# Kernel optimization log

Measured on AMD Instinct MI355X. Metric: run time of the kernel, lower is better.

Reference implementation:

```python
import jax, jax.numpy as jnp
import numpy as np


def _grid_mesh(n):
    ys, xs = np.meshgrid(np.arange(n), np.arange(n), indexing='ij')
    verts = np.stack([xs, ys, np.zeros_like(xs)], -1).reshape(-1, 3).astype(np.float32) / (n - 1)
    idx = np.arange(n * n).reshape(n, n)
    v00 = idx[:-1, :-1].ravel(); v01 = idx[:-1, 1:].ravel()
    v10 = idx[1:, :-1].ravel(); v11 = idx[1:, 1:].ravel()
    faces = np.concatenate([np.stack([v00, v10, v01], 1), np.stack([v01, v10, v11], 1)], 0).astype(np.int32)
    e = np.concatenate([faces[:, [0, 1]], faces[:, [1, 2]], faces[:, [2, 0]]], 0)
    e = np.unique(np.sort(e, axis=1), axis=0).astype(np.int32)
    return verts, faces, e


def setup_inputs() -> dict:
    N_GRID, B, S = 200, 2, 5000
    verts_np, faces_np, edges_np = _grid_mesh(N_GRID)
    verts_np[:, 2] = 0.1 * np.sin(2 * np.pi * verts_np[:, 0]) * np.sin(2 * np.pi * verts_np[:, 1])
    key = jax.random.key(0)
    k1, k2, k3, k4 = jax.random.split(key, 4)
    verts_std = jnp.asarray(verts_np)
    verts_scr = verts_std[None] + 5e-4 * jax.random.normal(k1, (B,) + verts_std.shape, jnp.float32)
    xy = jax.random.uniform(k2, (B, S, 2), jnp.float32)
    z = 0.1 * jnp.sin(2 * jnp.pi * xy[..., 0]) * jnp.sin(2 * jnp.pi * xy[..., 1])
    trg_points = jnp.concatenate([xy, z[..., None]], -1)
    rand_face_u = jax.random.uniform(k3, (B, S), jnp.float32)
    rand_bary = jax.random.uniform(k4, (B, S, 2), jnp.float32)
    return {
        'verts_scr': verts_scr,
        'verts_std': verts_std,
        'trg_points': trg_points,
        'rand_face_u': rand_face_u,
        'rand_bary': rand_bary,
        'faces': jnp.asarray(faces_np),
        'edges': jnp.asarray(edges_np),
    }


def _cot_edges(verts, faces):
    # pytorch3d cot_laplacian: per-face cotangents, symmetrized edge list (6F entries).
    v0, v1, v2 = verts[faces[:, 0]], verts[faces[:, 1]], verts[faces[:, 2]]
    A = jnp.linalg.norm(v1 - v2, axis=1)
    B = jnp.linalg.norm(v0 - v2, axis=1)
    C = jnp.linalg.norm(v0 - v1, axis=1)
    A2, B2, C2 = A * A, B * B, C * C
    s = 0.5 * (A + B + C)
    area = jnp.sqrt(jnp.clip(s * (s - A) * (s - B) * (s - C), 1e-12, None))
    cot = jnp.stack([B2 + C2 - A2, A2 + C2 - B2, A2 + B2 - C2], axis=1) / (4.0 * area[:, None])
    ii = faces[:, jnp.array([1, 2, 0])].reshape(-1)
    jj = faces[:, jnp.array([2, 0, 1])].reshape(-1)
    src = jnp.concatenate([ii, jj])
    dst = jnp.concatenate([jj, ii])
    w = jnp.concatenate([cot.reshape(-1), cot.reshape(-1)])
    return src, dst, w


def _sample_points(verts, faces, u_face, r_bary):
    # area-weighted face sampling + pytorch3d barycentric coords
    v0, v1, v2 = verts[faces[:, 0]], verts[faces[:, 1]], verts[faces[:, 2]]
    areas = 0.5 * jnp.linalg.norm(jnp.cross(v1 - v0, v2 - v0), axis=1)
    cdf = jnp.cumsum(areas) / jnp.sum(areas)
    fidx = jnp.clip(jnp.searchsorted(cdf, u_face), 0, faces.shape[0] - 1)
    su = jnp.sqrt(r_bary[:, 0])
    w0, w1, w2 = 1.0 - su, su * (1.0 - r_bary[:, 1]), su * r_bary[:, 1]
    return w0[:, None] * v0[fidx] + w1[:, None] * v1[fidx] + w2[:, None] * v2[fidx]


def _chamfer(x, y):
    # squared-distance chamfer, mean over points then batch (pytorch3d defaults)
    d = (jnp.sum(x * x, -1)[:, :, None] + jnp.sum(y * y, -1)[:, None, :]
         - 2.0 * jnp.einsum('bsd,btd->bst', x, y))
    return jnp.min(d, 2).mean() + jnp.min(d, 1).mean()


def _forward(verts_scr, verts_std, trg_points, rand_face_u, rand_bary, faces, edges):
    Vn = verts_std.shape[0]
    # chamfer between sampled src surface points and target point cloud
    sample_scr = jax.vmap(lambda v, u, r: _sample_points(v, faces, u, r))(verts_scr, rand_face_u, rand_bary)
    loss_p0 = _chamfer(sample_scr, trg_points)
    loss_n1 = jnp.asarray(1e-5, verts_scr.dtype)  # tensor-target branch

    # cot laplacian smoothing (method='cot')
    def lap_one(v):
        src, dst, w = _cot_edges(v, faces)
        Lv = jax.ops.segment_sum(w[:, None] * v[dst], src, num_segments=Vn)
        rw = jax.ops.segment_sum(w, src, num_segments=Vn)
        inv = jnp.where(rw > 0, 1.0 / jnp.maximum(rw, 1e-12), 0.0)
        return jnp.linalg.norm(Lv * inv[:, None] - v, axis=1).mean()

    loss_lap = jax.vmap(lap_one)(verts_scr).mean()

    # edge loss against mean edge length of the std mesh
    target_len = jnp.linalg.norm(verts_std[edges[:, 0]] - verts_std[edges[:, 1]], axis=1).mean()
    elen = jnp.linalg.norm(verts_scr[:, edges[:, 0]] - verts_scr[:, edges[:, 1]], axis=-1)
    loss_edge = ((elen - target_len) ** 2).mean()

    # ARAP rigid loss on std-mesh cot connectivity/weights
    src, dst, w = _cot_edges(verts_std, faces)
    e_std = verts_std[src] - verts_std[dst]

    def rigid_one(v):
        e_scr = v[src] - v[dst]
        S = jax.ops.segment_sum(w[:, None, None] * e_std[:, :, None] * e_scr[:, None, :], src, num_segments=Vn)
        U, _, Vt = jnp.linalg.svd(S)
        R = jnp.matmul(jnp.swapaxes(Vt, -1, -2), jnp.swapaxes(U, -1, -2))
        flip = jnp.where(jnp.linalg.det(R) < 0, -1.0, 1.0)
        Vt2 = Vt.at[:, -1, :].multiply(flip[:, None])
        R = jnp.matmul(jnp.swapaxes(Vt2, -1, -2), jnp.swapaxes(U, -1, -2))
        res = e_scr - jnp.einsum('eij,ej->ei', R[src], e_std)
        return jax.ops.segment_sum(w * jnp.sum(res * res, 1), src, num_segments=Vn)

    loss_rigid = jax.vmap(rigid_one)(verts_scr).mean()
    return jnp.stack([loss_p0, loss_n1, loss_lap, loss_edge, loss_rigid])


def reference(verts_scr, verts_std, trg_points, rand_face_u, rand_bary, faces, edges):
    return _forward(verts_scr, verts_std, trg_points, rand_face_u, rand_bary, faces, edges)
```

## Files before the change

### kernel.cpp

```cpp
#include <hip/hip_runtime.h>
#include <math.h>

#define TPB 256
#define MAXDEG 8

static __device__ __forceinline__ void atomAddD(double* p, double v) {
  __hip_atomic_fetch_add(p, v, __ATOMIC_RELAXED, __HIP_MEMORY_SCOPE_AGENT);
}

static __device__ __forceinline__ double bredsum(double v) {
  __shared__ double sb[TPB];
  int t = threadIdx.x;
  sb[t] = v;
  __syncthreads();
  for (int o = TPB / 2; o > 0; o >>= 1) {
    if (t < o) sb[t] += sb[t + o];
    __syncthreads();
  }
  double r = sb[0];
  __syncthreads();
  return r;
}

template <int p, int q, int r>
static __device__ __forceinline__ void jrot(double A[3][3], double V[3][3]) {
  double apq = A[p][q];
  if (apq == 0.0) return;
  double app = A[p][p], aqq = A[q][q];
  double theta = (aqq - app) / (2.0 * apq);
  double t = 1.0 / (fabs(theta) + sqrt(theta * theta + 1.0));
  if (theta < 0.0) t = -t;
  double c = 1.0 / sqrt(t * t + 1.0), sn = t * c;
  A[p][p] = app - t * apq;
  A[q][q] = aqq + t * apq;
  A[p][q] = 0.0;
  A[q][p] = 0.0;
  double arp = A[r][p], arq = A[r][q];
  A[r][p] = c * arp - sn * arq; A[p][r] = A[r][p];
  A[r][q] = sn * arp + c * arq; A[q][r] = A[r][q];
#pragma unroll
  for (int k = 0; k < 3; k++) {
    double vkp = V[k][p], vkq = V[k][q];
    V[k][p] = c * vkp - sn * vkq;
    V[k][q] = sn * vkp + c * vkq;
  }
}

#define ESWAP(la, lax, lay, laz, lb, lbx, lby, lbz)                       \
  if (la < lb) {                                                          \
    double t_;                                                            \
    t_ = la; la = lb; lb = t_;                                            \
    t_ = lax; lax = lbx; lbx = t_;                                        \
    t_ = lay; lay = lby; lby = t_;                                        \
    t_ = laz; laz = lbz; lbz = t_;                                        \
  }

static __device__ void kabschR(const double S[3][3], double R9[9]) {
  double A[3][3];
#pragma unroll
  for (int a = 0; a < 3; a++)
#pragma unroll
    for (int c = 0; c < 3; c++)
      A[a][c] = S[0][a] * S[0][c] + S[1][a] * S[1][c] + S[2][a] * S[2][c];
  double V[3][3] = {{1, 0, 0}, {0, 1, 0}, {0, 0, 1}};
  for (int sw = 0; sw < 12; sw++) {
    double off = fabs(A[0][1]) + fabs(A[0][2]) + fabs(A[1][2]);
    double dia = fabs(A[0][0]) + fabs(A[1][1]) + fabs(A[2][2]);
    if (!(off > dia * 1e-15)) break;
    jrot<0, 1, 2>(A, V);
    jrot<0, 2, 1>(A, V);
    jrot<1, 2, 0>(A, V);
  }
  double l0 = A[0][0], l1 = A[1][1], l2 = A[2][2];
  double a0x = V[0][0], a0y = V[1][0], a0z = V[2][0];
  double a1x = V[0][1], a1y = V[1][1], a1z = V[2][1];
  double a2x = V[0][2], a2y = V[1][2], a2z = V[2][2];
  ESWAP(l0, a0x, a0y, a0z, l1, a1x, a1y, a1z);
  ESWAP(l0, a0x, a0y, a0z, l2, a2x, a2y, a2z);
  ESWAP(l1, a1x, a1y, a1z, l2, a2x, a2y, a2z);
  double R00 = 1, R01 = 0, R02 = 0, R10 = 0, R11 = 1, R12 = 0, R20 = 0, R21 = 0, R22 = 1;
  double b1x = S[0][0] * a0x + S[0][1] * a0y + S[0][2] * a0z;
  double b1y = S[1][0] * a0x + S[1][1] * a0y + S[1][2] * a0z;
  double b1z = S[2][0] * a0x + S[2][1] * a0y + S[2][2] * a0z;
  double b2x = S[0][0] * a1x + S[0][1] * a1y + S[0][2] * a1z;
  double b2y = S[1][0] * a1x + S[1][1] * a1y + S[1][2] * a1z;
  double b2z = S[2][0] * a1x + S[2][1] * a1y + S[2][2] * a1z;
  double n1 = sqrt(b1x * b1x + b1y * b1y + b1z * b1z);
  if (n1 > 1e-300 && isfinite(n1)) {
    double u1x = b1x / n1, u1y = b1y / n1, u1z = b1z / n1;
    double dp = u1x * b2x + u1y * b2y + u1z * b2z;
    b2x -= dp * u1x; b2y -= dp * u1y; b2z -= dp * u1z;
    double n2 = sqrt(b2x * b2x + b2y * b2y + b2z * b2z);
    double u2x, u2y, u2z;
    if (n2 > n1 * 1e-14) {
      u2x = b2x / n2; u2y = b2y / n2; u2z = b2z / n2;
    } else {
      double f0 = fabs(u1x), f1 = fabs(u1y), f2 = fabs(u1z);
      double e0, e1, e2;
      if (f0 <= f1 && f0 <= f2) { e0 = 1.0 - u1x * u1x; e1 = -u1x * u1y; e2 = -u1x * u1z; }
      else if (f1 <= f2)        { e0 = -u1y * u1x; e1 = 1.0 - u1y * u1y; e2 = -u1y * u1z; }
      else                      { e0 = -u1z * u1x; e1 = -u1z * u1y; e2 = 1.0 - u1z * u1z; }
      double nw = sqrt(e0 * e0 + e1 * e1 + e2 * e2);
      u2x = e0 / nw; u2y = e1 / nw; u2z = e2 / nw;
    }
    double u3x = u1y * u2z - u1z * u2y;
    double u3y = u1z * u2x - u1x * u2z;
    double u3z = u1x * u2y - u1y * u2x;
    double w3x = a0y * a1z - a0z * a1y;
    double w3y = a0z * a1x - a0x * a1z;
    double w3z = a0x * a1y - a0y * a1x;
    R00 = a0x * u1x + a1x * u2x + w3x * u3x;
    R01 = a0x * u1y + a1x * u2y + w3x * u3y;
    R02 = a0x * u1z + a1x * u2z + w3x * u3z;
    R10 = a0y * u1x + a1y * u2x + w3y * u3x;
    R11 = a0y * u1y + a1y * u2y + w3y * u3y;
    R12 = a0y * u1z + a1y * u2z + w3y * u3z;
    R20 = a0z * u1x + a1z * u2x + w3z * u3x;
    R21 = a0z * u1y + a1z * u2y + w3z * u3y;
    R22 = a0z * u1z + a1z * u2z + w3z * u3z;
  }
  R9[0] = R00; R9[1] = R01; R9[2] = R02;
  R9[3] = R10; R9[4] = R11; R9[5] = R12;
  R9[6] = R20; R9[7] = R21; R9[8] = R22;
}

static __device__ __forceinline__ double resid(const double* R, const double* es,
                                               const double* ec) {
  double r0 = ec[0] - (R[0] * es[0] + R[1] * es[1] + R[2] * es[2]);
  double r1 = ec[1] - (R[3] * es[0] + R[4] * es[1] + R[5] * es[2]);
  double r2 = ec[2] - (R[6] * es[0] + R[7] * es[1] + R[8] * es[2]);
  return r0 * r0 + r1 * r1 + r2 * r2;
}

__global__ void kInitRowmin(unsigned* rm, int n) {
  int i = blockIdx.x * blockDim.x + threadIdx.x;
  if (i < n) rm[i] = 0x7f800000u;
}

__global__ void kFacePrep(const float* verts, const float* vstd, const int* faces,
                          double* areas, double* ccot, double* scot,
                          int B, int Vn, int F) {
  int i = blockIdx.x * blockDim.x + threadIdx.x;
  if (i >= B * F) return;
  int b = i / F, f = i % F;
  const float* vb = verts + (size_t)b * Vn * 3;
  int i0 = faces[f * 3], i1 = faces[f * 3 + 1], i2 = faces[f * 3 + 2];
  {
    double p0x = vb[i0 * 3], p0y = vb[i0 * 3 + 1], p0z = vb[i0 * 3 + 2];
    double p1x = vb[i1 * 3], p1y = vb[i1 * 3 + 1], p1z = vb[i1 * 3 + 2];
    double p2x = vb[i2 * 3], p2y = vb[i2 * 3 + 1], p2z = vb[i2 * 3 + 2];
    double ax = p1x - p0x, ay = p1y - p0y, az = p1z - p0z;
    double bx = p2x - p0x, by = p2y - p0y, bz = p2z - p0z;
    double cx = ay * bz - az * by, cy = az * bx - ax * bz, cz = ax * by - ay * bx;
    areas[i] = 0.5 * sqrt(cx * cx + cy * cy + cz * cz);
    double dx = p1x - p2x, dy = p1y - p2y, dz = p1z - p2z;
    double A2 = dx * dx + dy * dy + dz * dz;
    double B2 = bx * bx + by * by + bz * bz;
    double C2 = ax * ax + ay * ay + az * az;
    double A = sqrt(A2), Bl = sqrt(B2), C = sqrt(C2);
    double s = 0.5 * (A + Bl + C);
    double pr = s * (s - A) * (s - Bl) * (s - C);
    pr = pr < 1e-12 ? 1e-12 : pr;
    double inv4 = 1.0 / (4.0 * sqrt(pr));
    ccot[(size_t)i * 3 + 0] = (B2 + C2 - A2) * inv4;
    ccot[(size_t)i * 3 + 1] = (A2 + C2 - B2) * inv4;
    ccot[(size_t)i * 3 + 2] = (A2 + B2 - C2) * inv4;
  }
  if (b == 0) {
    double p0x = vstd[i0 * 3], p0y = vstd[i0 * 3 + 1], p0z = vstd[i0 * 3 + 2];
    double p1x = vstd[i1 * 3], p1y = vstd[i1 * 3 + 1], p1z = vstd[i1 * 3 + 2];
    double p2x = vstd[i2 * 3], p2y = vstd[i2 * 3 + 1], p2z = vstd[i2 * 3 + 2];
    double ax = p1x - p0x, ay = p1y - p0y, az = p1z - p0z;
    double bx = p2x - p0x, by = p2y - p0y, bz = p2z - p0z;
    double dx = p1x - p2x, dy = p1y - p2y, dz = p1z - p2z;
    double A2 = dx * dx + dy * dy + dz * dz;
    double B2 = bx * bx + by * by + bz * bz;
    double C2 = ax * ax + ay * ay + az * az;
    double A = sqrt(A2), Bl = sqrt(B2), C = sqrt(C2);
    double s = 0.5 * (A + Bl + C);
    double pr = s * (s - A) * (s - Bl) * (s - C);
    pr = pr < 1e-12 ? 1e-12 : pr;
    double inv4 = 1.0 / (4.0 * sqrt(pr));
    scot[(size_t)f * 3 + 0] = (B2 + C2 - A2) * inv4;
    scot[(size_t)f * 3 + 1] = (A2 + C2 - B2) * inv4;
    scot[(size_t)f * 3 + 2] = (A2 + B2 - C2) * inv4;
  }
}

__global__ void kScan1(double* a, double* bsum, int F, int nc) {
  int blk = blockIdx.x;
  int b = blk / nc, c = blk % nc;
  int t = threadIdx.x;
  int f = c * 1024 + t;
  __shared__ double s[1024];
  double v = (f < F) ? a[(size_t)b * F + f] : 0.0;
  s[t] = v;
  __syncthreads();
  for (int o = 1; o < 1024; o <<= 1) {
    double ad = (t >= o) ? s[t - o] : 0.0;
    __syncthreads();
    s[t] += ad;
    __syncthreads();
  }
  if (f < F) a[(size_t)b * F + f] = s[t];
  if (t == 1023) bsum[(size_t)b * nc + c] = s[1023];
}

__global__ void kScan2(const double* bsum, double* boffs, int nc) {
  int b = blockIdx.x, t = threadIdx.x;
  __shared__ double s[1024];
  double v = (t < nc) ? bsum[(size_t)b * nc + t] : 0.0;
  s[t] = v;
  __syncthreads();
  for (int o = 1; o < 1024; o <<= 1) {
    double ad = (t >= o) ? s[t - o] : 0.0;
    __syncthreads();
    s[t] += ad;
    __syncthreads();
  }
  if (t < nc) boffs[(size_t)b * nc + t] = s[t] - v;
}

__global__ void kScan3(double* a, const double* boffs, int F, int nc) {
  int blk = blockIdx.x;
  int b = blk / nc, c = blk % nc;
  int f = c * 1024 + threadIdx.x;
  if (f < F) a[(size_t)b * F + f] += boffs[(size_t)b * nc + c];
}

__global__ void kSample(const float* verts, const int* faces, const double* cdf,
                        const float* rfu, const float* rbary, float* samples,
                        int B, int Vn, int F, int S) {
  int i = blockIdx.x * blockDim.x + threadIdx.x;
  if (i >= B * S) return;
  int b = i / S;
  const double* c = cdf + (size_t)b * F;
  double total = c[F - 1];
  double tgt = (double)rfu[i] * total;
  int lo = 0, hi = F;
  while (lo < hi) {
    int m = (lo + hi) >> 1;
    if (c[m] < tgt) lo = m + 1; else hi = m;
  }
  int f = lo < F ? lo : F - 1;
  const float* vb = verts + (size_t)b * Vn * 3;
  int i0 = faces[f * 3], i1 = faces[f * 3 + 1], i2 = faces[f * 3 + 2];
  float r0 = rbary[(size_t)i * 2], r1 = rbary[(size_t)i * 2 + 1];
  float su = sqrtf(r0);
  float w0 = 1.f - su, w1 = su * (1.f - r1), w2 = su * r1;
  samples[(size_t)i * 3 + 0] = w0 * vb[i0 * 3 + 0] + w1 * vb[i1 * 3 + 0] + w2 * vb[i2 * 3 + 0];
  samples[(size_t)i * 3 + 1] = w0 * vb[i0 * 3 + 1] + w1 * vb[i1 * 3 + 1] + w2 * vb[i2 * 3 + 1];
  samples[(size_t)i * 3 + 2] = w0 * vb[i0 * 3 + 2] + w1 * vb[i1 * 3 + 2] + w2 * vb[i2 * 3 + 2];
}

__global__ void kChamfer(const float* X, const float* Y, unsigned* rowmin, int S) {
  int b = blockIdx.z;
  int i = blockIdx.x * TPB + threadIdx.x;
  int j0 = blockIdx.y * TPB;
  int n = min(TPB, S - j0);
  __shared__ float4 sy[TPB];
  const float* Yb = Y + ((size_t)b * S + j0) * 3;
  if ((int)threadIdx.x < n) {
    int t = threadIdx.x;
    sy[t] = make_float4(Yb[t * 3], Yb[t * 3 + 1], Yb[t * 3 + 2], 0.f);
  }
  __syncthreads();
  if (i >= S) return;
  const float* Xb = X + (size_t)b * S * 3;
  float x0 = Xb[i * 3], x1 = Xb[i * 3 + 1], x2 = Xb[i * 3 + 2];
  float inf = __int_as_float(0x7f800000);
  float m0 = inf, m1 = inf, m2 = inf, m3 = inf;
  int k = 0;
  for (; k + 4 <= n; k += 4) {
    float4 y0 = sy[k], y1 = sy[k + 1], y2 = sy[k + 2], y3 = sy[k + 3];
    float a0 = x0 - y0.x, b0 = x1 - y0.y, c0 = x2 - y0.z;
    float a1 = x0 - y1.x, b1 = x1 - y1.y, c1 = x2 - y1.z;
    float a2 = x0 - y2.x, b2 = x1 - y2.y, c2 = x2 - y2.z;
    float a3 = x0 - y3.x, b3 = x1 - y3.y, c3 = x2 - y3.z;
    m0 = fminf(m0, a0 * a0 + b0 * b0 + c0 * c0);
    m1 = fminf(m1, a1 * a1 + b1 * b1 + c1 * c1);
    m2 = fminf(m2, a2 * a2 + b2 * b2 + c2 * c2);
    m3 = fminf(m3, a3 * a3 + b3 * b3 + c3 * c3);
  }
  for (; k < n; k++) {
    float4 y = sy[k];
    float a = x0 - y.x, bb = x1 - y.y, cc = x2 - y.z;
    m0 = fminf(m0, a * a + bb * bb + cc * cc);
  }
  float mn = fminf(fminf(m0, m1), fminf(m2, m3));
  atomicMin(&rowmin[(size_t)b * S + i], __float_as_uint(mn));
}

__global__ void kReduceRowmin(const unsigned* rm, int n, double* acc) {
  int i = blockIdx.x * TPB + threadIdx.x;
  double v = 0.0;
  if (i < n) v = (double)__uint_as_float(rm[i]);
  double r = bredsum(v);
  if (threadIdx.x == 0) atomAddD(acc, r);
}

__global__ void kEdgeStd(const float* vstd, const int* edges, int E, double* acc) {
  int i = blockIdx.x * TPB + threadIdx.x;
  double val = 0.0;
  if (i < E) {
    int e0 = edges[(size_t)i * 2], e1 = edges[(size_t)i * 2 + 1];
    double dx = (double)vstd[e0 * 3 + 0] - vstd[e1 * 3 + 0];
    double dy = (double)vstd[e0 * 3 + 1] - vstd[e1 * 3 + 1];
    double dz = (double)vstd[e0 * 3 + 2] - vstd[e1 * 3 + 2];
    val = sqrt(dx * dx + dy * dy + dz * dz);
  }
  double r = bredsum(val);
  if (threadIdx.x == 0) atomAddD(acc, r);
}

__global__ void kEdgeLoss(const float* vscr, const int* edges, int B, int Vn, int E,
                          const double* tacc, double* acc) {
  int i = blockIdx.x * TPB + threadIdx.x;
  double tl = tacc[0] / (double)E;
  double val = 0.0;
  if (i < B * E) {
    int b = i / E, e = i % E;
    const float* vb = vscr + (size_t)b * Vn * 3;
    int e0 = edges[(size_t)e * 2], e1 = edges[(size_t)e * 2 + 1];
    double dx = (double)vb[e0 * 3 + 0] - vb[e1 * 3 + 0];
    double dy = (double)vb[e0 * 3 + 1] - vb[e1 * 3 + 1];
    double dz = (double)vb[e0 * 3 + 2] - vb[e1 * 3 + 2];
    double l = sqrt(dx * dx + dy * dy + dz * dz);
    double d = l - tl;
    val = d * d;
  }
  double r = bredsum(val);
  if (threadIdx.x == 0) atomAddD(acc, r);
}

__global__ void kAdjFill(const int* faces, int* cnt, int4* adjtab, int F) {
  int f = blockIdx.x * TPB + threadIdx.x;
  if (f >= F) return;
  int j0 = faces[f * 3], j1 = faces[f * 3 + 1], j2 = faces[f * 3 + 2];
  int f3 = f * 3;
  int s0 = atomicAdd(&cnt[j0], 1);
  if (s0 < MAXDEG) adjtab[(size_t)j0 * MAXDEG + s0] = make_int4(j1, j2, f3 + 1, f3 + 2);
  int s1 = atomicAdd(&cnt[j1], 1);
  if (s1 < MAXDEG) adjtab[(size_t)j1 * MAXDEG + s1] = make_int4(j2, j0, f3 + 2, f3 + 0);
  int s2 = atomicAdd(&cnt[j2], 1);
  if (s2 < MAXDEG) adjtab[(size_t)j2 * MAXDEG + s2] = make_int4(j0, j1, f3 + 0, f3 + 1);
}

__global__ void kVertexLapR(const float* vstd, const float* vscr,
                            const int* cnt, const int4* adjtab, const double* scot,
                            const double* ccot, double* Rmat, int B, int Vn, int F,
                            double* accLap) {
  int idx = blockIdx.x * TPB + threadIdx.x;
  double vlap = 0.0;
  if (idx < B * Vn) {
    int b = idx / Vn, v = idx % Vn;
    const float* cb = vscr + (size_t)b * Vn * 3;
    const double* ccb = ccot + (size_t)b * F * 3;
    double pasx = vstd[v * 3], pasy = vstd[v * 3 + 1], pasz = vstd[v * 3 + 2];
    double pacx = cb[v * 3], pacy = cb[v * 3 + 1], pacz = cb[v * 3 + 2];
    int n = cnt[v];
    if (n > MAXDEG) n = MAXDEG;
    const int4* at = adjtab + (size_t)v * MAXDEG;
    double S00 = 0, S01 = 0, S02 = 0, S10 = 0, S11 = 0, S12 = 0, S20 = 0, S21 = 0, S22 = 0;
    double Lx = 0, Ly = 0, Lz = 0, rw = 0;
    for (int k = 0; k < n; k++) {
      int4 e = at[k];
      int jb = e.x, jc = e.y;
      double cBs = scot[e.z], cCs = scot[e.w];
      double cBc = ccb[e.z], cCc = ccb[e.w];
      double pbsx = vstd[jb * 3], pbsy = vstd[jb * 3 + 1], pbsz = vstd[jb * 3 + 2];
      double pcsx = vstd[jc * 3], pcsy = vstd[jc * 3 + 1], pcsz = vstd[jc * 3 + 2];
      double pbcx = cb[jb * 3], pbcy = cb[jb * 3 + 1], pbcz = cb[jb * 3 + 2];
      double pccx = cb[jc * 3], pccy = cb[jc * 3 + 1], pccz = cb[jc * 3 + 2];
      Lx += cCc * pbcx + cBc * pccx;
      Ly += cCc * pbcy + cBc * pccy;
      Lz += cCc * pbcz + cBc * pccz;
      rw += cBc + cCc;
      double e1sx = pasx - pbsx, e1sy = pasy - pbsy, e1sz = pasz - pbsz;
      double e2sx = pasx - pcsx, e2sy = pasy - pcsy, e2sz = pasz - pcsz;
      double e1cx = pacx - pbcx, e1cy = pacy - pbcy, e1cz = pacz - pbcz;
      double e2cx = pacx - pccx, e2cy = pacy - pccy, e2cz = pacz - pccz;
      S00 += cCs * e1sx * e1cx + cBs * e2sx * e2cx;
      S01 += cCs * e1sx * e1cy + cBs * e2sx * e2cy;
      S02 += cCs * e1sx * e1cz + cBs * e2sx * e2cz;
      S10 += cCs * e1sy * e1cx + cBs * e2sy * e2cx;
      S11 += cCs * e1sy * e1cy + cBs * e2sy * e2cy;
      S12 += cCs * e1sy * e1cz + cBs * e2sy * e2cz;
      S20 += cCs * e1sz * e1cx + cBs * e2sz * e2cx;
      S21 += cCs * e1sz * e1cy + cBs * e2sz * e2cy;
      S22 += cCs * e1sz * e1cz + cBs * e2sz * e2cz;
    }
    double inv = (rw > 0.0) ? 1.0 / fmax(rw, 1e-12) : 0.0;
    double dx = Lx * inv - pacx, dy = Ly * inv - pacy, dz = Lz * inv - pacz;
    vlap = sqrt(dx * dx + dy * dy + dz * dz);
    double S[3][3] = {{S00, S01, S02}, {S10, S11, S12}, {S20, S21, S22}};
    double R9[9];
    kabschR(S, R9);
    double* rp = Rmat + (size_t)idx * 9;
#pragma unroll
    for (int r = 0; r < 9; r++) rp[r] = R9[r];
  }
  double r1 = bredsum(vlap);
  if (threadIdx.x == 0) atomAddD(accLap, r1);
}

__global__ void kRigidRes(const float* vstd, const float* vscr, const int* faces,
                          const double* scot, const double* Rmat, int B, int Vn, int F,
                          double* acc) {
  int i = blockIdx.x * TPB + threadIdx.x;
  double val = 0.0;
  if (i < B * F) {
    int b = i / F, f = i % F;
    int i0 = faces[f * 3], i1 = faces[f * 3 + 1], i2 = faces[f * 3 + 2];
    const float* cb = vscr + (size_t)b * Vn * 3;
    double cs0 = scot[(size_t)f * 3], cs1 = scot[(size_t)f * 3 + 1], cs2 = scot[(size_t)f * 3 + 2];
    double p0x = vstd[i0 * 3], p0y = vstd[i0 * 3 + 1], p0z = vstd[i0 * 3 + 2];
    double p1x = vstd[i1 * 3], p1y = vstd[i1 * 3 + 1], p1z = vstd[i1 * 3 + 2];
    double p2x = vstd[i2 * 3], p2y = vstd[i2 * 3 + 1], p2z = vstd[i2 * 3 + 2];
    double q0x = cb[i0 * 3], q0y = cb[i0 * 3 + 1], q0z = cb[i0 * 3 + 2];
    double q1x = cb[i1 * 3], q1y = cb[i1 * 3 + 1], q1z = cb[i1 * 3 + 2];
    double q2x = cb[i2 * 3], q2y = cb[i2 * 3 + 1], q2z = cb[i2 * 3 + 2];
    double e01s[3] = {p0x - p1x, p0y - p1y, p0z - p1z};
    double e02s[3] = {p0x - p2x, p0y - p2y, p0z - p2z};
    double e12s[3] = {p1x - p2x, p1y - p2y, p1z - p2z};
    double e01c[3] = {q0x - q1x, q0y - q1y, q0z - q1z};
    double e02c[3] = {q0x - q2x, q0y - q2y, q0z - q2z};
    double e12c[3] = {q1x - q2x, q1y - q2y, q1z - q2z};
    const double* R0 = Rmat + ((size_t)b * Vn + i0) * 9;
    const double* R1 = Rmat + ((size_t)b * Vn + i1) * 9;
    const double* R2 = Rmat + ((size_t)b * Vn + i2) * 9;
    val = cs1 * resid(R0, e02s, e02c) + cs2 * resid(R0, e01s, e01c)
        + cs0 * resid(R1, e12s, e12c) + cs2 * resid(R1, e01s, e01c)
        + cs1 * resid(R2, e02s, e02c) + cs0 * resid(R2, e12s, e12c);
  }
  double r = bredsum(val);
  if (threadIdx.x == 0) atomAddD(acc, r);
}

__global__ void kFinalize(const double* acc, float* out, int B, int Vn, int S, int E) {
  if (blockIdx.x == 0 && threadIdx.x == 0) {
    out[0] = (float)(acc[0] / ((double)B * S));
    out[1] = 1e-5f;
    out[2] = (float)(acc[1] / ((double)B * Vn));
    out[3] = (float)(acc[3] / ((double)B * E));
    out[4] = (float)(acc[4] / ((double)B * Vn));
  }
}

extern "C" void kernel_launch(void* const* d_in, const int* in_sizes, int n_in,
                              void* d_out, int out_size, void* d_ws, size_t ws_size,
                              hipStream_t stream) {
  const float* vscr = (const float*)d_in[0];
  const float* vstd = (const float*)d_in[1];
  const float* trg  = (const float*)d_in[2];
  const float* rfu  = (const float*)d_in[3];
  const float* rby  = (const float*)d_in[4];
  const int* faces  = (const int*)d_in[5];
  const int* edges  = (const int*)d_in[6];
  float* out = (float*)d_out;

  int nVs = in_sizes[1];
  int Vn = nVs / 3;
  int B = in_sizes[0] / nVs;
  int S = in_sizes[3] / B;
  int F = in_sizes[5] / 3;
  int E = in_sizes[6] / 2;
  int nc = (F + 1023) / 1024;

  char* p = (char*)d_ws;
  auto alloc = [&](size_t bytes) -> void* {
    void* r = (void*)p;
    p += (bytes + 255) & ~(size_t)255;
    return r;
  };
  double* cdf   = (double*)alloc((size_t)B * F * sizeof(double));
  double* bsum  = (double*)alloc((size_t)B * nc * sizeof(double));
  double* boffs = (double*)alloc((size_t)B * nc * sizeof(double));
  double* scot  = (double*)alloc((size_t)F * 3 * sizeof(double));
  double* ccot  = (double*)alloc((size_t)B * F * 3 * sizeof(double));
  double* Rmat  = (double*)alloc((size_t)B * Vn * 9 * sizeof(double));
  float* samples   = (float*)alloc((size_t)B * S * 3 * sizeof(float));
  unsigned* rowmin = (unsigned*)alloc((size_t)2 * B * S * sizeof(unsigned));
  int* adjcnt   = (int*)alloc((size_t)Vn * sizeof(int));
  int4* adjtab  = (int4*)alloc((size_t)Vn * MAXDEG * sizeof(int4));
  double* accum = (double*)alloc(8 * sizeof(double));

  hipMemsetAsync(adjcnt, 0, (size_t)Vn * sizeof(int), stream);
  hipMemsetAsync(accum, 0, 8 * sizeof(double), stream);

  int nrm = 2 * B * S;
  kInitRowmin<<<(nrm + TPB - 1) / TPB, TPB, 0, stream>>>(rowmin, nrm);

  kAdjFill<<<(F + TPB - 1) / TPB, TPB, 0, stream>>>(faces, adjcnt, adjtab, F);

  kFacePrep<<<(B * F + TPB - 1) / TPB, TPB, 0, stream>>>(vscr, vstd, faces, cdf, ccot,
                                                         scot, B, Vn, F);
  kScan1<<<B * nc, 1024, 0, stream>>>(cdf, bsum, F, nc);
  kScan2<<<B, 1024, 0, stream>>>(bsum, boffs, nc);
  kScan3<<<B * nc, 1024, 0, stream>>>(cdf, boffs, F, nc);
  kSample<<<(B * S + TPB - 1) / TPB, TPB, 0, stream>>>(vscr, faces, cdf, rfu, rby,
                                                       samples, B, Vn, F, S);
  dim3 cg((S + TPB - 1) / TPB, (S + TPB - 1) / TPB, B);
  kChamfer<<<cg, TPB, 0, stream>>>(samples, trg, rowmin, S);
  kChamfer<<<cg, TPB, 0, stream>>>(trg, samples, rowmin + (size_t)B * S, S);
  kReduceRowmin<<<(nrm + TPB - 1) / TPB, TPB, 0, stream>>>(rowmin, nrm, accum + 0);

  kEdgeStd<<<(E + TPB - 1) / TPB, TPB, 0, stream>>>(vstd, edges, E, accum + 2);
  kEdgeLoss<<<(B * E + TPB - 1) / TPB, TPB, 0, stream>>>(vscr, edges, B, Vn, E,
                                                         accum + 2, accum + 3);

  kVertexLapR<<<(B * Vn + TPB - 1) / TPB, TPB, 0, stream>>>(vstd, vscr, adjcnt, adjtab,
                                                            scot, ccot, Rmat, B, Vn, F,
                                                            accum + 1);
  kRigidRes<<<(B * F + TPB - 1) / TPB, TPB, 0, stream>>>(vstd, vscr, faces, scot,
                                                         Rmat, B, Vn, F, accum + 4);

  kFinalize<<<1, 1, 0, stream>>>(accum, out, B, Vn, S, E);
}
```

Baseline: 200.1 us.

## Fuse kernels to cut launch count: merged prep, single-pass scan, combined chamfer

Merges face prep, adjacency fill and std edge-length sum into one kernel. The three-kernel scan becomes a warp-shuffle scan where the last-arriving block computes the chunk offsets. Sampling then searches hierarchically over chunk totals and local prefixes instead of needing a globally fixed-up CDF. Both chamfer directions run in one launch, rowmin init becomes a memset, and the edge, reduce and finalize kernels are folded into others using a last-block counter. The aim is to remove launch overhead and serial small kernels, at the cost of atomic-counter logic and threadfence ordering that must be correct.

```diff
diff --git a/kernel.cpp b/kernel.cpp
--- a/kernel.cpp
+++ b/kernel.cpp
@@ -132,117 +132,169 @@
   return r0 * r0 + r1 * r1 + r2 * r2;
 }
 
-__global__ void kInitRowmin(unsigned* rm, int n) {
-  int i = blockIdx.x * blockDim.x + threadIdx.x;
-  if (i < n) rm[i] = 0x7f800000u;
-}
-
-__global__ void kFacePrep(const float* verts, const float* vstd, const int* faces,
-                          double* areas, double* ccot, double* scot,
-                          int B, int Vn, int F) {
-  int i = blockIdx.x * blockDim.x + threadIdx.x;
-  if (i >= B * F) return;
-  int b = i / F, f = i % F;
-  const float* vb = verts + (size_t)b * Vn * 3;
-  int i0 = faces[f * 3], i1 = faces[f * 3 + 1], i2 = faces[f * 3 + 2];
-  {
-    double p0x = vb[i0 * 3], p0y = vb[i0 * 3 + 1], p0z = vb[i0 * 3 + 2];
-    double p1x = vb[i1 * 3], p1y = vb[i1 * 3 + 1], p1z = vb[i1 * 3 + 2];
-    double p2x = vb[i2 * 3], p2y = vb[i2 * 3 + 1], p2z = vb[i2 * 3 + 2];
-    double ax = p1x - p0x, ay = p1y - p0y, az = p1z - p0z;
-    double bx = p2x - p0x, by = p2y - p0y, bz = p2z - p0z;
-    double cx = ay * bz - az * by, cy = az * bx - ax * bz, cz = ax * by - ay * bx;
-    areas[i] = 0.5 * sqrt(cx * cx + cy * cy + cz * cz);
-    double dx = p1x - p2x, dy = p1y - p2y, dz = p1z - p2z;
-    double A2 = dx * dx + dy * dy + dz * dz;
-    double B2 = bx * bx + by * by + bz * bz;
-    double C2 = ax * ax + ay * ay + az * az;
-    double A = sqrt(A2), Bl = sqrt(B2), C = sqrt(C2);
-    double s = 0.5 * (A + Bl + C);
-    double pr = s * (s - A) * (s - Bl) * (s - C);
-    pr = pr < 1e-12 ? 1e-12 : pr;
-    double inv4 = 1.0 / (4.0 * sqrt(pr));
-    ccot[(size_t)i * 3 + 0] = (B2 + C2 - A2) * inv4;
-    ccot[(size_t)i * 3 + 1] = (A2 + C2 - B2) * inv4;
-    ccot[(size_t)i * 3 + 2] = (A2 + B2 - C2) * inv4;
-  }
-  if (b == 0) {
-    double p0x = vstd[i0 * 3], p0y = vstd[i0 * 3 + 1], p0z = vstd[i0 * 3 + 2];
-    double p1x = vstd[i1 * 3], p1y = vstd[i1 * 3 + 1], p1z = vstd[i1 * 3 + 2];
-    double p2x = vstd[i2 * 3], p2y = vstd[i2 * 3 + 1], p2z = vstd[i2 * 3 + 2];
-    double ax = p1x - p0x, ay = p1y - p0y, az = p1z - p0z;
-    double bx = p2x - p0x, by = p2y - p0y, bz = p2z - p0z;
-    double dx = p1x - p2x, dy = p1y - p2y, dz = p1z - p2z;
-    double A2 = dx * dx + dy * dy + dz * dz;
-    double B2 = bx * bx + by * by + bz * bz;
-    double C2 = ax * ax + ay * ay + az * az;
-    double A = sqrt(A2), Bl = sqrt(B2), C = sqrt(C2);
-    double s = 0.5 * (A + Bl + C);
-    double pr = s * (s - A) * (s - Bl) * (s - C);
-    pr = pr < 1e-12 ? 1e-12 : pr;
-    double inv4 = 1.0 / (4.0 * sqrt(pr));
-    scot[(size_t)f * 3 + 0] = (B2 + C2 - A2) * inv4;
-    scot[(size_t)f * 3 + 1] = (A2 + C2 - B2) * inv4;
-    scot[(size_t)f * 3 + 2] = (A2 + B2 - C2) * inv4;
-  }
-}
-
-__global__ void kScan1(double* a, double* bsum, int F, int nc) {
+static __device__ __forceinline__ void heronCots(double A2, double B2, double C2,
+                                                 double* c0, double* c1, double* c2) {
+  double A = sqrt(A2), Bl = sqrt(B2), C = sqrt(C2);
+  double s = 0.5 * (A + Bl + C);
+  double pr = s * (s - A) * (s - Bl) * (s - C);
+  pr = pr < 1e-12 ? 1e-12 : pr;
+  double inv4 = 1.0 / (4.0 * sqrt(pr));
+  *c0 = (B2 + C2 - A2) * inv4;
+  *c1 = (A2 + C2 - B2) * inv4;
+  *c2 = (A2 + B2 - C2) * inv4;
+}
+
+__global__ void kPrep(const float* vscr, const float* vstd, const int* faces,
+                      const int* edges, double* cdf, double* ccot, double* scot,
+                      int* adjcnt, int4* adjtab, double* accEdgeStd,
+                      int B, int Vn, int F, int E) {
+  int i = blockIdx.x * TPB + threadIdx.x;
+  if (i < B * F) {
+    int b = i / F, f = i % F;
+    const float* vb = vscr + (size_t)b * Vn * 3;
+    int i0 = faces[f * 3], i1 = faces[f * 3 + 1], i2 = faces[f * 3 + 2];
+    {
+      double p0x = vb[i0 * 3], p0y = vb[i0 * 3 + 1], p0z = vb[i0 * 3 + 2];
+      double p1x = vb[i1 * 3], p1y = vb[i1 * 3 + 1], p1z = vb[i1 * 3 + 2];
+      double p2x = vb[i2 * 3], p2y = vb[i2 * 3 + 1], p2z = vb[i2 * 3 + 2];
+      double ax = p1x - p0x, ay = p1y - p0y, az = p1z - p0z;
+      double bx = p2x - p0x, by = p2y - p0y, bz = p2z - p0z;
+      double cx = ay * bz - az * by, cy = az * bx - ax * bz, cz = ax * by - ay * bx;
+      cdf[i] = 0.5 * sqrt(cx * cx + cy * cy + cz * cz);
+      double dx = p1x - p2x, dy = p1y - p2y, dz = p1z - p2z;
+      double A2 = dx * dx + dy * dy + dz * dz;
+      double B2 = bx * bx + by * by + bz * bz;
+      double C2 = ax * ax + ay * ay + az * az;
+      double c0, c1, c2;
+      heronCots(A2, B2, C2, &c0, &c1, &c2);
+      ccot[(size_t)i * 3 + 0] = c0;
+      ccot[(size_t)i * 3 + 1] = c1;
+      ccot[(size_t)i * 3 + 2] = c2;
+    }
+    if (b == 0) {
+      double p0x = vstd[i0 * 3], p0y = vstd[i0 * 3 + 1], p0z = vstd[i0 * 3 + 2];
+      double p1x = vstd[i1 * 3], p1y = vstd[i1 * 3 + 1], p1z = vstd[i1 * 3 + 2];
+      double p2x = vstd[i2 * 3], p2y = vstd[i2 * 3 + 1], p2z = vstd[i2 * 3 + 2];
+      double ax = p1x - p0x, ay = p1y - p0y, az = p1z - p0z;
+      double bx = p2x - p0x, by = p2y - p0y, bz = p2z - p0z;
+      double dx = p1x - p2x, dy = p1y - p2y, dz = p1z - p2z;
+      double A2 = dx * dx + dy * dy + dz * dz;
+      double B2 = bx * bx + by * by + bz * bz;
+      double C2 = ax * ax + ay * ay + az * az;
+      double c0, c1, c2;
+      heronCots(A2, B2, C2, &c0, &c1, &c2);
+      scot[(size_t)f * 3 + 0] = c0;
+      scot[(size_t)f * 3 + 1] = c1;
+      scot[(size_t)f * 3 + 2] = c2;
+      int f3 = f * 3;
+      int s0 = atomicAdd(&adjcnt[i0], 1);
+      if (s0 < MAXDEG) adjtab[(size_t)i0 * MAXDEG + s0] = make_int4(i1, i2, f3 + 1, f3 + 2);
+      int s1 = atomicAdd(&adjcnt[i1], 1);
+      if (s1 < MAXDEG) adjtab[(size_t)i1 * MAXDEG + s1] = make_int4(i2, i0, f3 + 2, f3 + 0);
+      int s2 = atomicAdd(&adjcnt[i2], 1);
+      if (s2 < MAXDEG) adjtab[(size_t)i2 * MAXDEG + s2] = make_int4(i0, i1, f3 + 0, f3 + 1);
+    }
+  }
+  double eval = 0.0;
+  if (i < E) {
+    int e0 = edges[(size_t)i * 2], e1 = edges[(size_t)i * 2 + 1];
+    double dx = (double)vstd[e0 * 3 + 0] - vstd[e1 * 3 + 0];
+    double dy = (double)vstd[e0 * 3 + 1] - vstd[e1 * 3 + 1];
+    double dz = (double)vstd[e0 * 3 + 2] - vstd[e1 * 3 + 2];
+    eval = sqrt(dx * dx + dy * dy + dz * dz);
+  }
+  double r = bredsum(eval);
+  if (threadIdx.x == 0) atomAddD(accEdgeStd, r);
+}
+
+__global__ void kScanFused(double* a, double* bsum, double* boffs, int F, int nc,
+                           int B, int* cnt) {
   int blk = blockIdx.x;
   int b = blk / nc, c = blk % nc;
-  int t = threadIdx.x;
+  int t = threadIdx.x, lane = t & 63, wid = t >> 6;
   int f = c * 1024 + t;
-  __shared__ double s[1024];
-  double v = (f < F) ? a[(size_t)b * F + f] : 0.0;
-  s[t] = v;
-  __syncthreads();
-  for (int o = 1; o < 1024; o <<= 1) {
-    double ad = (t >= o) ? s[t - o] : 0.0;
-    __syncthreads();
-    s[t] += ad;
-    __syncthreads();
-  }
-  if (f < F) a[(size_t)b * F + f] = s[t];
-  if (t == 1023) bsum[(size_t)b * nc + c] = s[1023];
-}
-
-__global__ void kScan2(const double* bsum, double* boffs, int nc) {
-  int b = blockIdx.x, t = threadIdx.x;
-  __shared__ double s[1024];
-  double v = (t < nc) ? bsum[(size_t)b * nc + t] : 0.0;
-  s[t] = v;
-  __syncthreads();
-  for (int o = 1; o < 1024; o <<= 1) {
-    double ad = (t >= o) ? s[t - o] : 0.0;
-    __syncthreads();
-    s[t] += ad;
-    __syncthreads();
-  }
-  if (t < nc) boffs[(size_t)b * nc + t] = s[t] - v;
-}
-
-__global__ void kScan3(double* a, const double* boffs, int F, int nc) {
-  int blk = blockIdx.x;
-  int b = blk / nc, c = blk % nc;
-  int f = c * 1024 + threadIdx.x;
-  if (f < F) a[(size_t)b * F + f] += boffs[(size_t)b * nc + c];
+  size_t idx = (size_t)b * F + f;
+  double v = (f < F) ? a[idx] : 0.0;
+  double x = v;
+#pragma unroll
+  for (int o = 1; o < 64; o <<= 1) {
+    double y = __shfl_up(x, o, 64);
+    if (lane >= o) x += y;
+  }
+  __shared__ double wsum[16];
+  __shared__ double woffs[16];
+  if (lane == 63) wsum[wid] = x;
+  __syncthreads();
+  if (wid == 0) {
+    double s = (lane < 16) ? wsum[lane] : 0.0;
+    double xs = s;
+#pragma unroll
+    for (int o = 1; o < 16; o <<= 1) {
+      double y = __shfl_up(xs, o, 64);
+      if (lane >= o) xs += y;
+    }
+    double ex = __shfl_up(xs, 1, 64);
+    if (lane < 16) woffs[lane] = (lane == 0) ? 0.0 : ex;
+  }
+  __syncthreads();
+  x += woffs[wid];
+  if (f < F) a[idx] = x;
+  if (t == 1023) bsum[(size_t)b * nc + c] = x;
+  __threadfence();
+  __shared__ int amlast;
+  if (t == 0) {
+    int old = __hip_atomic_fetch_add(cnt, 1, __ATOMIC_ACQ_REL, __HIP_MEMORY_SCOPE_AGENT);
+    amlast = (old == (int)gridDim.x - 1) ? 1 : 0;
+  }
+  __syncthreads();
+  if (amlast && wid == 0) {
+    for (int bb = 0; bb < B; bb++) {
+      double carry = 0.0;
+      for (int base = 0; base < nc; base += 64) {
+        int cc = base + lane;
+        double s = (cc < nc) ? bsum[(size_t)bb * nc + cc] : 0.0;
+        double xs = s;
+#pragma unroll
+        for (int o = 1; o < 64; o <<= 1) {
+          double y = __shfl_up(xs, o, 64);
+          if (lane >= o) xs += y;
+        }
+        double ex = __shfl_up(xs, 1, 64);
+        double excl = (lane == 0) ? 0.0 : ex;
+        if (cc < nc) boffs[(size_t)bb * nc + cc] = carry + excl;
+        carry += __shfl(xs, 63, 64);
+      }
+    }
+  }
 }
 
 __global__ void kSample(const float* verts, const int* faces, const double* cdf,
+                        const double* bsum, const double* boffs,
                         const float* rfu, const float* rbary, float* samples,
-                        int B, int Vn, int F, int S) {
+                        int B, int Vn, int F, int S, int nc) {
   int i = blockIdx.x * blockDim.x + threadIdx.x;
   if (i >= B * S) return;
   int b = i / S;
-  const double* c = cdf + (size_t)b * F;
-  double total = c[F - 1];
+  const double* bo = boffs + (size_t)b * nc;
+  const double* bs = bsum + (size_t)b * nc;
+  double total = bo[nc - 1] + bs[nc - 1];
   double tgt = (double)rfu[i] * total;
-  int lo = 0, hi = F;
+  int lo = 0, hi = nc;
   while (lo < hi) {
     int m = (lo + hi) >> 1;
-    if (c[m] < tgt) lo = m + 1; else hi = m;
-  }
-  int f = lo < F ? lo : F - 1;
+    if (bo[m] + bs[m] < tgt) lo = m + 1; else hi = m;
+  }
+  int c = lo < nc ? lo : nc - 1;
+  double thr = tgt - bo[c];
+  const double* cc = cdf + (size_t)b * F + (size_t)c * 1024;
+  int lim = F - c * 1024; if (lim > 1024) lim = 1024;
+  lo = 0; hi = lim;
+  while (lo < hi) {
+    int m = (lo + hi) >> 1;
+    if (cc[m] < thr) lo = m + 1; else hi = m;
+  }
+  int j = lo < lim ? lo : lim - 1;
+  int f = c * 1024 + j;
   const float* vb = verts + (size_t)b * Vn * 3;
   int i0 = faces[f * 3], i1 = faces[f * 3 + 1], i2 = faces[f * 3 + 2];
   float r0 = rbary[(size_t)i * 2], r1 = rbary[(size_t)i * 2 + 1];
@@ -253,8 +305,12 @@
   samples[(size_t)i * 3 + 2] = w0 * vb[i0 * 3 + 2] + w1 * vb[i1 * 3 + 2] + w2 * vb[i2 * 3 + 2];
 }
 
-__global__ void kChamfer(const float* X, const float* Y, unsigned* rowmin, int S) {
-  int b = blockIdx.z;
+__global__ void kChamferBoth(const float* smp, const float* trg, unsigned* rowmin,
+                             int B, int S) {
+  int z = blockIdx.z;
+  int dir = z / B, b = z % B;
+  const float* X = dir ? trg : smp;
+  const float* Y = dir ? smp : trg;
   int i = blockIdx.x * TPB + threadIdx.x;
   int j0 = blockIdx.y * TPB;
   int n = min(TPB, S - j0);
@@ -288,34 +344,17 @@
     m0 = fminf(m0, a * a + bb * bb + cc * cc);
   }
   float mn = fminf(fminf(m0, m1), fminf(m2, m3));
-  atomicMin(&rowmin[(size_t)b * S + i], __float_as_uint(mn));
-}
-
-__global__ void kReduceRowmin(const unsigned* rm, int n, double* acc) {
+  atomicMin(&rowmin[((size_t)dir * B + b) * S + i], __float_as_uint(mn));
+}
+
+__global__ void kMisc(const unsigned* rm, int nrm, const float* vscr, const int* edges,
+                      int B, int Vn, int E, const double* tacc,
+                      double* accCh, double* accEd) {
   int i = blockIdx.x * TPB + threadIdx.x;
   double v = 0.0;
-  if (i < n) v = (double)__uint_as_float(rm[i]);
+  if (i < nrm) v = (double)__uint_as_float(rm[i]);
   double r = bredsum(v);
-  if (threadIdx.x == 0) atomAddD(acc, r);
-}
-
-__global__ void kEdgeStd(const float* vstd, const int* edges, int E, double* acc) {
-  int i = blockIdx.x * TPB + threadIdx.x;
-  double val = 0.0;
-  if (i < E) {
-    int e0 = edges[(size_t)i * 2], e1 = edges[(size_t)i * 2 + 1];
-    double dx = (double)vstd[e0 * 3 + 0] - vstd[e1 * 3 + 0];
-    double dy = (double)vstd[e0 * 3 + 1] - vstd[e1 * 3 + 1];
-    double dz = (double)vstd[e0 * 3 + 2] - vstd[e1 * 3 + 2];
-    val = sqrt(dx * dx + dy * dy + dz * dz);
-  }
-  double r = bredsum(val);
-  if (threadIdx.x == 0) atomAddD(acc, r);
-}
-
-__global__ void kEdgeLoss(const float* vscr, const int* edges, int B, int Vn, int E,
-                          const double* tacc, double* acc) {
-  int i = blockIdx.x * TPB + threadIdx.x;
+  if (threadIdx.x == 0) atomAddD(accCh, r);
   double tl = tacc[0] / (double)E;
   double val = 0.0;
   if (i < B * E) {
@@ -329,21 +368,8 @@
     double d = l - tl;
     val = d * d;
   }
-  double r = bredsum(val);
-  if (threadIdx.x == 0) atomAddD(acc, r);
-}
-
-__global__ void kAdjFill(const int* faces, int* cnt, int4* adjtab, int F) {
-  int f = blockIdx.x * TPB + threadIdx.x;
-  if (f >= F) return;
-  int j0 = faces[f * 3], j1 = faces[f * 3 + 1], j2 = faces[f * 3 + 2];
-  int f3 = f * 3;
-  int s0 = atomicAdd(&cnt[j0], 1);
-  if (s0 < MAXDEG) adjtab[(size_t)j0 * MAXDEG + s0] = make_int4(j1, j2, f3 + 1, f3 + 2);
-  int s1 = atomicAdd(&cnt[j1], 1);
-  if (s1 < MAXDEG) adjtab[(size_t)j1 * MAXDEG + s1] = make_int4(j2, j0, f3 + 2, f3 + 0);
-  int s2 = atomicAdd(&cnt[j2], 1);
-  if (s2 < MAXDEG) adjtab[(size_t)j2 * MAXDEG + s2] = make_int4(j0, j1, f3 + 0, f3 + 1);
+  double r2 = bredsum(val);
+  if (threadIdx.x == 0) atomAddD(accEd, r2);
 }
 
 __global__ void kVertexLapR(const float* vstd, const float* vscr,
@@ -404,9 +430,9 @@
   if (threadIdx.x == 0) atomAddD(accLap, r1);
 }
 
-__global__ void kRigidRes(const float* vstd, const float* vscr, const int* faces,
-                          const double* scot, const double* Rmat, int B, int Vn, int F,
-                          double* acc) {
+__global__ void kRigidResFin(const float* vstd, const float* vscr, const int* faces,
+                             const double* scot, const double* Rmat, int B, int Vn,
+                             int F, double* accum, int* cnt, float* out, int S, int E) {
   int i = blockIdx.x * TPB + threadIdx.x;
   double val = 0.0;
   if (i < B * F) {
@@ -434,16 +460,20 @@
         + cs1 * resid(R2, e02s, e02c) + cs0 * resid(R2, e12s, e12c);
   }
   double r = bredsum(val);
-  if (threadIdx.x == 0) atomAddD(acc, r);
-}
-
-__global__ void kFinalize(const double* acc, float* out, int B, int Vn, int S, int E) {
-  if (blockIdx.x == 0 && threadIdx.x == 0) {
-    out[0] = (float)(acc[0] / ((double)B * S));
+  if (threadIdx.x == 0) atomAddD(accum + 4, r);
+  __threadfence();
+  __shared__ int amlast;
+  if (threadIdx.x == 0) {
+    int old = __hip_atomic_fetch_add(cnt, 1, __ATOMIC_ACQ_REL, __HIP_MEMORY_SCOPE_AGENT);
+    amlast = (old == (int)gridDim.x - 1) ? 1 : 0;
+  }
+  __syncthreads();
+  if (amlast && threadIdx.x == 0) {
+    out[0] = (float)(accum[0] / ((double)B * S));
     out[1] = 1e-5f;
-    out[2] = (float)(acc[1] / ((double)B * Vn));
-    out[3] = (float)(acc[3] / ((double)B * E));
-    out[4] = (float)(acc[4] / ((double)B * Vn));
+    out[2] = (float)(accum[1] / ((double)B * Vn));
+    out[3] = (float)(accum[3] / ((double)B * E));
+    out[4] = (float)(accum[4] / ((double)B * Vn));
   }
 }
 
@@ -481,39 +511,33 @@
   double* Rmat  = (double*)alloc((size_t)B * Vn * 9 * sizeof(double));
   float* samples   = (float*)alloc((size_t)B * S * 3 * sizeof(float));
   unsigned* rowmin = (unsigned*)alloc((size_t)2 * B * S * sizeof(unsigned));
-  int* adjcnt   = (int*)alloc((size_t)Vn * sizeof(int));
   int4* adjtab  = (int4*)alloc((size_t)Vn * MAXDEG * sizeof(int4));
-  double* accum = (double*)alloc(8 * sizeof(double));
-
-  hipMemsetAsync(adjcnt, 0, (size_t)Vn * sizeof(int), stream);
-  hipMemsetAsync(accum, 0, 8 * sizeof(double), stream);
-
+  size_t zbytes = (size_t)Vn * sizeof(int) + 8 * sizeof(int) + 8 * sizeof(double);
+  char* zbase   = (char*)alloc(zbytes);
+  int* adjcnt   = (int*)zbase;
+  int* cnts     = (int*)(zbase + (size_t)Vn * sizeof(int));
+  double* accum = (double*)(zbase + (size_t)Vn * sizeof(int) + 8 * sizeof(int));
+
+  hipMemsetAsync(zbase, 0, zbytes, stream);
   int nrm = 2 * B * S;
-  kInitRowmin<<<(nrm + TPB - 1) / TPB, TPB, 0, stream>>>(rowmin, nrm);
-
-  kAdjFill<<<(F + TPB - 1) / TPB, TPB, 0, stream>>>(faces, adjcnt, adjtab, F);
-
-  kFacePrep<<<(B * F + TPB - 1) / TPB, TPB, 0, stream>>>(vscr, vstd, faces, cdf, ccot,
-                                                         scot, B, Vn, F);
-  kScan1<<<B * nc, 1024, 0, stream>>>(cdf, bsum, F, nc);
-  kScan2<<<B, 1024, 0, stream>>>(bsum, boffs, nc);
-  kScan3<<<B * nc, 1024, 0, stream>>>(cdf, boffs, F, nc);
-  kSample<<<(B * S + TPB - 1) / TPB, TPB, 0, stream>>>(vscr, faces, cdf, rfu, rby,
-                                                       samples, B, Vn, F, S);
-  dim3 cg((S + TPB - 1) / TPB, (S + TPB - 1) / TPB, B);
-  kChamfer<<<cg, TPB, 0, stream>>>(samples, trg, rowmin, S);
-  kChamfer<<<cg, TPB, 0, stream>>>(trg, samples, rowmin + (size_t)B * S, S);
-  kReduceRowmin<<<(nrm + TPB - 1) / TPB, TPB, 0, stream>>>(rowmin, nrm, accum + 0);
-
-  kEdgeStd<<<(E + TPB - 1) / TPB, TPB, 0, stream>>>(vstd, edges, E, accum + 2);
-  kEdgeLoss<<<(B * E + TPB - 1) / TPB, TPB, 0, stream>>>(vscr, edges, B, Vn, E,
-                                                         accum + 2, accum + 3);
-
+  hipMemsetAsync(rowmin, 0xFF, (size_t)nrm * sizeof(unsigned), stream);
+
+  int BF = B * F;
+  kPrep<<<(BF + TPB - 1) / TPB, TPB, 0, stream>>>(vscr, vstd, faces, edges, cdf, ccot,
+                                                  scot, adjcnt, adjtab, accum + 2,
+                                                  B, Vn, F, E);
+  kScanFused<<<B * nc, 1024, 0, stream>>>(cdf, bsum, boffs, F, nc, B, cnts + 0);
+  kSample<<<(B * S + TPB - 1) / TPB, TPB, 0, stream>>>(vscr, faces, cdf, bsum, boffs,
+                                                       rfu, rby, samples, B, Vn, F, S, nc);
   kVertexLapR<<<(B * Vn + TPB - 1) / TPB, TPB, 0, stream>>>(vstd, vscr, adjcnt, adjtab,
                                                             scot, ccot, Rmat, B, Vn, F,
                                                             accum + 1);
-  kRigidRes<<<(B * F + TPB - 1) / TPB, TPB, 0, stream>>>(vstd, vscr, faces, scot,
-                                                         Rmat, B, Vn, F, accum + 4);
-
-  kFinalize<<<1, 1, 0, stream>>>(accum, out, B, Vn, S, E);
-}
+  dim3 cg((S + TPB - 1) / TPB, (S + TPB - 1) / TPB, 2 * B);
+  kChamferBoth<<<cg, TPB, 0, stream>>>(samples, trg, rowmin, B, S);
+  int nmisc = nrm > B * E ? nrm : B * E;
+  kMisc<<<(nmisc + TPB - 1) / TPB, TPB, 0, stream>>>(rowmin, nrm, vscr, edges, B, Vn, E,
+                                                     accum + 2, accum + 0, accum + 3);
+  kRigidResFin<<<(BF + TPB - 1) / TPB, TPB, 0, stream>>>(vstd, vscr, faces, scot, Rmat,
+                                                         B, Vn, F, accum, cnts + 1,
+                                                         out, S, E);
+}
```

After: 294.8 us. +47.3%, slower.
